# Performance work log

Measured on AMD Instinct MI355X. Metric: run time of the kernel, lower is better.

## Reference

```python
import jax, jax.numpy as jnp
import numpy as np

B, NCAP, LEN, CDF = 8, 4, 1024, 768
NUM, IDF = 1024, 512


def setup_inputs() -> dict:
    key = jax.random.key(0)
    k1, k2, k3 = jax.random.split(key, 3)
    obj = jax.random.normal(k1, (B, NUM, IDF), dtype=jnp.float32)
    text = jax.random.normal(k2, (B, NCAP, LEN, CDF), dtype=jnp.float32)
    # Linear(cdf=768 -> idf=512); kaiming-uniform-ish scale
    W = jax.random.normal(k3, (CDF, IDF), dtype=jnp.float32) / np.sqrt(CDF)
    b = jnp.zeros((IDF,), dtype=jnp.float32)
    return {"obj": obj, "text": text, "W": W, "b": b}


def reference(obj, text, W, b):
    # obj: [B, num, idf]; text: [B, 4, len, cdf]
    batch = text.shape[0]
    idf = obj.shape[2]
    # conv_context: Linear(cdf -> idf), then flatten captions: [B, L=4*len, idf]
    t = (jnp.einsum('bcle,ed->bcld', text, W) + b).reshape(batch, -1, idf)
    # unscaled, unmasked cross-attention scores: [B, num, L]
    attn = jnp.einsum('bnd,bld->bnl', obj, t)
    # softmax over the flattened text dim (nn.Softmax on 2D applies to last dim)
    attn = jax.nn.softmax(attn, axis=-1)
    # dropout(p=0.5) is identity in eval mode (deterministic reference)
    # weightedText = bmm(t^T, attn^T) then transpose -> [B, num, idf]
    out = jnp.einsum('bnl,bld->bnd', attn, t)
    return out
```

## Files before the change

kernel.cpp:

```cpp
#include <hip/hip_runtime.h>
#include <math.h>


typedef unsigned short u16;
typedef u16   u16x4  __attribute__((ext_vector_type(4)));
typedef u16   u16x8  __attribute__((ext_vector_type(8)));
typedef __bf16 bf16x8 __attribute__((ext_vector_type(8)));
typedef float f32x4  __attribute__((ext_vector_type(4)));

__device__ inline u16 f32_to_bf16_rne(float x) {
  unsigned u = __builtin_bit_cast(unsigned, x);
  return (u16)((u + 0x7FFFu + ((u >> 16) & 1u)) >> 16);
}
__device__ inline float bf16_to_f32(u16 h) {
  return __builtin_bit_cast(float, (unsigned)h << 16);
}

template<bool ADD_BIAS>
__global__ __launch_bounds__(256, 2) void gemm_nt_bf16x3(
    const float* __restrict__ A, const float* __restrict__ B,
    float* __restrict__ C, const float* __restrict__ bias,
    int M, int N, int K, long sA, long sB, long sC)
{
  __shared__ __align__(16) u16 Ah[128][40];
  __shared__ __align__(16) u16 Al[128][40];
  __shared__ __align__(16) u16 Bh[128][40];
  __shared__ __align__(16) u16 Bl[128][40];

  const float* Ab = A + (long)blockIdx.z * sA;
  const float* Bb = B + (long)blockIdx.z * sB;
  float*       Cb = C + (long)blockIdx.z * sC;

  const int m0 = blockIdx.y * 128;
  const int n0 = blockIdx.x * 128;
  const int t    = threadIdx.x;
  const int lane = t & 63;
  const int w    = t >> 6;
  const int wm   = w >> 1;
  const int wn   = w & 1;
  const int lr   = lane & 15;
  const int lg   = lane >> 4;

  f32x4 acc[4][4];
  #pragma unroll
  for (int i = 0; i < 4; i++)
    #pragma unroll
    for (int j = 0; j < 4; j++) acc[i][j] = (f32x4){0.f, 0.f, 0.f, 0.f};

  for (int k0 = 0; k0 < K; k0 += 32) {
    float4 av[4], bv[4];
    #pragma unroll
    for (int i = 0; i < 4; i++) {
      const int f   = t + 256 * i;
      const int row = f >> 3;
      const int kq  = (f & 7) * 4;
      av[i] = *reinterpret_cast<const float4*>(Ab + (long)(m0 + row) * K + k0 + kq);
      bv[i] = *reinterpret_cast<const float4*>(Bb + (long)(n0 + row) * K + k0 + kq);
    }
    __syncthreads();
    #pragma unroll
    for (int i = 0; i < 4; i++) {
      const int f   = t + 256 * i;
      const int row = f >> 3;
      const int kq  = (f & 7) * 4;
      u16x4 ah4, al4, bh4, bl4;
      const float* ap = reinterpret_cast<const float*>(&av[i]);
      const float* bp = reinterpret_cast<const float*>(&bv[i]);
      #pragma unroll
      for (int c = 0; c < 4; c++) {
        u16 h = f32_to_bf16_rne(ap[c]);
        ah4[c] = h;
        al4[c] = f32_to_bf16_rne(ap[c] - bf16_to_f32(h));
        h = f32_to_bf16_rne(bp[c]);
        bh4[c] = h;
        bl4[c] = f32_to_bf16_rne(bp[c] - bf16_to_f32(h));
      }
      *reinterpret_cast<u16x4*>(&Ah[row][kq]) = ah4;
      *reinterpret_cast<u16x4*>(&Al[row][kq]) = al4;
      *reinterpret_cast<u16x4*>(&Bh[row][kq]) = bh4;
      *reinterpret_cast<u16x4*>(&Bl[row][kq]) = bl4;
    }
    __syncthreads();

    bf16x8 afh[4], afl[4], bfh[4], bfl[4];
    #pragma unroll
    for (int i = 0; i < 4; i++) {
      const int ar = wm * 64 + i * 16 + lr;
      const int br = wn * 64 + i * 16 + lr;
      afh[i] = __builtin_bit_cast(bf16x8, *reinterpret_cast<const u16x8*>(&Ah[ar][lg * 8]));
      afl[i] = __builtin_bit_cast(bf16x8, *reinterpret_cast<const u16x8*>(&Al[ar][lg * 8]));
      bfh[i] = __builtin_bit_cast(bf16x8, *reinterpret_cast<const u16x8*>(&Bh[br][lg * 8]));
      bfl[i] = __builtin_bit_cast(bf16x8, *reinterpret_cast<const u16x8*>(&Bl[br][lg * 8]));
    }
    #pragma unroll
    for (int i = 0; i < 4; i++)
      #pragma unroll
      for (int j = 0; j < 4; j++) {
        acc[i][j] = __builtin_amdgcn_mfma_f32_16x16x32_bf16(afl[i], bfh[j], acc[i][j], 0, 0, 0);
        acc[i][j] = __builtin_amdgcn_mfma_f32_16x16x32_bf16(afh[i], bfl[j], acc[i][j], 0, 0, 0);
        acc[i][j] = __builtin_amdgcn_mfma_f32_16x16x32_bf16(afh[i], bfh[j], acc[i][j], 0, 0, 0);
      }
  }

  #pragma unroll
  for (int j = 0; j < 4; j++) {
    const int col = n0 + wn * 64 + j * 16 + lr;
    const float bj = ADD_BIAS ? bias[col] : 0.f;
    #pragma unroll
    for (int i = 0; i < 4; i++) {
      const int row = m0 + wm * 64 + i * 16 + lg * 4;
      #pragma unroll
      for (int r = 0; r < 4; r++)
        Cb[(long)(row + r) * N + col] = acc[i][j][r] + bj;
    }
  }
}

__global__ __launch_bounds__(256) void transpose_f32(
    const float* __restrict__ in, float* __restrict__ out,
    int R, int C, long sIn, long sOut)
{
  __shared__ float tile[32][33];
  in  += (long)blockIdx.z * sIn;
  out += (long)blockIdx.z * sOut;
  const int c  = blockIdx.x * 32 + threadIdx.x;
  const int r0 = blockIdx.y * 32 + threadIdx.y;
  #pragma unroll
  for (int j = 0; j < 32; j += 8)
    tile[threadIdx.y + j][threadIdx.x] = in[(long)(r0 + j) * C + c];
  __syncthreads();
  const int c2 = blockIdx.y * 32 + threadIdx.x;
  const int r2 = blockIdx.x * 32 + threadIdx.y;
  #pragma unroll
  for (int j = 0; j < 32; j += 8)
    out[(long)(r2 + j) * R + c2] = tile[threadIdx.x][threadIdx.y + j];
}

__device__ inline float wave_max(float x) {
  #pragma unroll
  for (int o = 1; o < 64; o <<= 1) x = fmaxf(x, __shfl_xor(x, o, 64));
  return x;
}
__device__ inline float wave_sum(float x) {
  #pragma unroll
  for (int o = 1; o < 64; o <<= 1) x += __shfl_xor(x, o, 64);
  return x;
}

__global__ __launch_bounds__(256) void softmax4096_kernel(float* __restrict__ attn)
{
  __shared__ float red[4];
  float* p = attn + (long)blockIdx.x * 4096;
  const int t = threadIdx.x;

  float4 v[4];
  float mx = -3.4e38f;
  #pragma unroll
  for (int i = 0; i < 4; i++) {
    v[i] = *reinterpret_cast<const float4*>(p + i * 1024 + t * 4);
    mx = fmaxf(mx, fmaxf(fmaxf(v[i].x, v[i].y), fmaxf(v[i].z, v[i].w)));
  }
  mx = wave_max(mx);
  if ((t & 63) == 0) red[t >> 6] = mx;
  __syncthreads();
  mx = fmaxf(fmaxf(red[0], red[1]), fmaxf(red[2], red[3]));
  __syncthreads();

  float s = 0.f;
  #pragma unroll
  for (int i = 0; i < 4; i++) {
    v[i].x = __expf(v[i].x - mx); s += v[i].x;
    v[i].y = __expf(v[i].y - mx); s += v[i].y;
    v[i].z = __expf(v[i].z - mx); s += v[i].z;
    v[i].w = __expf(v[i].w - mx); s += v[i].w;
  }
  s = wave_sum(s);
  if ((t & 63) == 0) red[t >> 6] = s;
  __syncthreads();
  const float r = 1.f / (red[0] + red[1] + red[2] + red[3]);

  #pragma unroll
  for (int i = 0; i < 4; i++) {
    v[i].x *= r; v[i].y *= r; v[i].z *= r; v[i].w *= r;
    *reinterpret_cast<float4*>(p + i * 1024 + t * 4) = v[i];
  }
}

extern "C" void kernel_launch(void* const* d_in, const int* in_sizes, int n_in,
                              void* d_out, int out_size, void* d_ws, size_t ws_size,
                              hipStream_t stream)
{
  const float* obj  = (const float*)d_in[0];
  const float* text = (const float*)d_in[1];
  const float* W    = (const float*)d_in[2];
  const float* bias = (const float*)d_in[3];
  float*       out  = (float*)d_out;

  float* t    = (float*)d_ws;
  float* attn = t    + 32768L * 512;
  float* tT   = attn + 8L * 1024 * 4096;
  float* WT   = tT   + 8L * 512 * 4096;

  transpose_f32<<<dim3(512 / 32, 768 / 32, 1), dim3(32, 8), 0, stream>>>(
      W, WT, 768, 512, 0L, 0L);
  gemm_nt_bf16x3<true><<<dim3(512 / 128, 32768 / 128, 1), 256, 0, stream>>>(
      text, WT, t, bias, 32768, 512, 768, 0L, 0L, 0L);
  transpose_f32<<<dim3(512 / 32, 4096 / 32, 8), dim3(32, 8), 0, stream>>>(
      t, tT, 4096, 512, 4096L * 512, 512L * 4096);
  gemm_nt_bf16x3<false><<<dim3(4096 / 128, 1024 / 128, 8), 256, 0, stream>>>(
      obj, t, attn, nullptr, 1024, 4096, 512,
      1024L * 512, 4096L * 512, 1024L * 4096);
  softmax4096_kernel<<<8192, 256, 0, stream>>>(attn);
  gemm_nt_bf16x3<false><<<dim3(512 / 128, 1024 / 128, 8), 256, 0, stream>>>(
      attn, tT, out, nullptr, 1024, 512, 4096,
      1024L * 4096, 512L * 4096, 1024L * 512);
}
```

Measured before the change: 681.1 us.

## Double-buffer LDS tiles and prefetch next K-tile during MFMA in bf16x3 GEMM

Turns the GEMM main loop into a software pipeline with two LDS buffers. The global loads for the next K-tile are issued before the current tile's MFMAs, and the split-convert-store into the other buffer happens afterwards, so each iteration needs one barrier instead of two. The hand-written bf16 rounding is replaced with native __bf16 casts, and B fragments are loaded per column to lower register pressure. LDS use doubles to about 80 KB per block, which may limit occupancy at the requested two blocks per CU.

```diff
diff --git a/kernel.cpp b/kernel.cpp
--- a/kernel.cpp
+++ b/kernel.cpp
@@ -8,12 +8,15 @@
 typedef __bf16 bf16x8 __attribute__((ext_vector_type(8)));
 typedef float f32x4  __attribute__((ext_vector_type(4)));
 
-__device__ inline u16 f32_to_bf16_rne(float x) {
-  unsigned u = __builtin_bit_cast(unsigned, x);
-  return (u16)((u + 0x7FFFu + ((u >> 16) & 1u)) >> 16);
-}
-__device__ inline float bf16_to_f32(u16 h) {
-  return __builtin_bit_cast(float, (unsigned)h << 16);
+__device__ inline void split4(const float4 v, u16x4* h4, u16x4* l4) {
+  const float xs[4] = {v.x, v.y, v.z, v.w};
+  #pragma unroll
+  for (int c = 0; c < 4; c++) {
+    __bf16 hb = (__bf16)xs[c];
+    __bf16 lb = (__bf16)(xs[c] - (float)hb);
+    (*h4)[c] = __builtin_bit_cast(u16, hb);
+    (*l4)[c] = __builtin_bit_cast(u16, lb);
+  }
 }
 
 template<bool ADD_BIAS>
@@ -22,10 +25,10 @@
     float* __restrict__ C, const float* __restrict__ bias,
     int M, int N, int K, long sA, long sB, long sC)
 {
-  __shared__ __align__(16) u16 Ah[128][40];
-  __shared__ __align__(16) u16 Al[128][40];
-  __shared__ __align__(16) u16 Bh[128][40];
-  __shared__ __align__(16) u16 Bl[128][40];
+  __shared__ __align__(16) u16 Ah[2][128][40];
+  __shared__ __align__(16) u16 Al[2][128][40];
+  __shared__ __align__(16) u16 Bh[2][128][40];
+  __shared__ __align__(16) u16 Bl[2][128][40];
 
   const float* Ab = A + (long)blockIdx.z * sA;
   const float* Bb = B + (long)blockIdx.z * sB;
@@ -47,60 +50,67 @@
     #pragma unroll
     for (int j = 0; j < 4; j++) acc[i][j] = (f32x4){0.f, 0.f, 0.f, 0.f};
 
-  for (int k0 = 0; k0 < K; k0 += 32) {
-    float4 av[4], bv[4];
-    #pragma unroll
-    for (int i = 0; i < 4; i++) {
-      const int f   = t + 256 * i;
-      const int row = f >> 3;
-      const int kq  = (f & 7) * 4;
-      av[i] = *reinterpret_cast<const float4*>(Ab + (long)(m0 + row) * K + k0 + kq);
-      bv[i] = *reinterpret_cast<const float4*>(Bb + (long)(n0 + row) * K + k0 + kq);
-    }
-    __syncthreads();
-    #pragma unroll
-    for (int i = 0; i < 4; i++) {
-      const int f   = t + 256 * i;
-      const int row = f >> 3;
-      const int kq  = (f & 7) * 4;
-      u16x4 ah4, al4, bh4, bl4;
-      const float* ap = reinterpret_cast<const float*>(&av[i]);
-      const float* bp = reinterpret_cast<const float*>(&bv[i]);
-      #pragma unroll
-      for (int c = 0; c < 4; c++) {
-        u16 h = f32_to_bf16_rne(ap[c]);
-        ah4[c] = h;
-        al4[c] = f32_to_bf16_rne(ap[c] - bf16_to_f32(h));
-        h = f32_to_bf16_rne(bp[c]);
-        bh4[c] = h;
-        bl4[c] = f32_to_bf16_rne(bp[c] - bf16_to_f32(h));
-      }
-      *reinterpret_cast<u16x4*>(&Ah[row][kq]) = ah4;
-      *reinterpret_cast<u16x4*>(&Al[row][kq]) = al4;
-      *reinterpret_cast<u16x4*>(&Bh[row][kq]) = bh4;
-      *reinterpret_cast<u16x4*>(&Bl[row][kq]) = bl4;
-    }
-    __syncthreads();
-
-    bf16x8 afh[4], afl[4], bfh[4], bfl[4];
+  float4 av[4], bv[4];
+
+  #define LOADK(K0)                                                                 \
+    _Pragma("unroll")                                                               \
+    for (int i = 0; i < 4; i++) {                                                   \
+      const int f   = t + 256 * i;                                                  \
+      const int row = f >> 3;                                                       \
+      const int kq  = (f & 7) * 4;                                                  \
+      av[i] = *reinterpret_cast<const float4*>(Ab + (long)(m0 + row) * K + (K0) + kq); \
+      bv[i] = *reinterpret_cast<const float4*>(Bb + (long)(n0 + row) * K + (K0) + kq); \
+    }
+
+  #define CONVWRITE(BUF)                                                            \
+    _Pragma("unroll")                                                               \
+    for (int i = 0; i < 4; i++) {                                                   \
+      const int f   = t + 256 * i;                                                  \
+      const int row = f >> 3;                                                       \
+      const int kq  = (f & 7) * 4;                                                  \
+      u16x4 h4, l4;                                                                 \
+      split4(av[i], &h4, &l4);                                                      \
+      *reinterpret_cast<u16x4*>(&Ah[BUF][row][kq]) = h4;                            \
+      *reinterpret_cast<u16x4*>(&Al[BUF][row][kq]) = l4;                            \
+      split4(bv[i], &h4, &l4);                                                      \
+      *reinterpret_cast<u16x4*>(&Bh[BUF][row][kq]) = h4;                            \
+      *reinterpret_cast<u16x4*>(&Bl[BUF][row][kq]) = l4;                            \
+    }
+
+  LOADK(0)
+  CONVWRITE(0)
+  __syncthreads();
+
+  const int nk = K >> 5;
+  for (int kt = 0; kt < nk; ++kt) {
+    const int cur = kt & 1;
+    if (kt + 1 < nk) { LOADK((kt + 1) << 5) }
+
+    bf16x8 afh[4], afl[4];
     #pragma unroll
     for (int i = 0; i < 4; i++) {
       const int ar = wm * 64 + i * 16 + lr;
-      const int br = wn * 64 + i * 16 + lr;
-      afh[i] = __builtin_bit_cast(bf16x8, *reinterpret_cast<const u16x8*>(&Ah[ar][lg * 8]));
-      afl[i] = __builtin_bit_cast(bf16x8, *reinterpret_cast<const u16x8*>(&Al[ar][lg * 8]));
-      bfh[i] = __builtin_bit_cast(bf16x8, *reinterpret_cast<const u16x8*>(&Bh[br][lg * 8]));
-      bfl[i] = __builtin_bit_cast(bf16x8, *reinterpret_cast<const u16x8*>(&Bl[br][lg * 8]));
-    }
-    #pragma unroll
-    for (int i = 0; i < 4; i++)
+      afh[i] = __builtin_bit_cast(bf16x8, *reinterpret_cast<const u16x8*>(&Ah[cur][ar][lg * 8]));
+      afl[i] = __builtin_bit_cast(bf16x8, *reinterpret_cast<const u16x8*>(&Al[cur][ar][lg * 8]));
+    }
+    #pragma unroll
+    for (int j = 0; j < 4; j++) {
+      const int br = wn * 64 + j * 16 + lr;
+      bf16x8 bh = __builtin_bit_cast(bf16x8, *reinterpret_cast<const u16x8*>(&Bh[cur][br][lg * 8]));
+      bf16x8 bl = __builtin_bit_cast(bf16x8, *reinterpret_cast<const u16x8*>(&Bl[cur][br][lg * 8]));
       #pragma unroll
-      for (int j = 0; j < 4; j++) {
-        acc[i][j] = __builtin_amdgcn_mfma_f32_16x16x32_bf16(afl[i], bfh[j], acc[i][j], 0, 0, 0);
-        acc[i][j] = __builtin_amdgcn_mfma_f32_16x16x32_bf16(afh[i], bfl[j], acc[i][j], 0, 0, 0);
-        acc[i][j] = __builtin_amdgcn_mfma_f32_16x16x32_bf16(afh[i], bfh[j], acc[i][j], 0, 0, 0);
+      for (int i = 0; i < 4; i++) {
+        acc[i][j] = __builtin_amdgcn_mfma_f32_16x16x32_bf16(afl[i], bh, acc[i][j], 0, 0, 0);
+        acc[i][j] = __builtin_amdgcn_mfma_f32_16x16x32_bf16(afh[i], bl, acc[i][j], 0, 0, 0);
+        acc[i][j] = __builtin_amdgcn_mfma_f32_16x16x32_bf16(afh[i], bh, acc[i][j], 0, 0, 0);
       }
-  }
+    }
+
+    if (kt + 1 < nk) { CONVWRITE(cur ^ 1) }
+    __syncthreads();
+  }
+  #undef LOADK
+  #undef CONVWRITE
 
   #pragma unroll
   for (int j = 0; j < 4; j++) {
```

New measurement: 557.8 us. -18.1%, faster.
